# Kernel optimization log

Measured on AMD Instinct MI355X. Metric: run time of the kernel, lower is better.

Reference implementation:

```python
import jax, jax.numpy as jnp
import numpy as np

B, S, D, H = 8, 512, 1024, 16
DH = D // H
GAMMA = 0.1      # kl_gamma
KL_EPS = 1e-10
LN_EPS = 1e-5
SCALE = 1.0 / np.sqrt(DH).astype(np.float32)


def setup_inputs() -> dict:
    key = jax.random.key(0)
    ks = iter(jax.random.split(key, 32))
    rnd = lambda shape, s: jax.random.normal(next(ks), shape, jnp.float32) * s
    inp = {
        'title_features': rnd((B, S, D), 1.0),
        'content_features': rnd((B, S, D), 1.0),
    }
    for pre in ('t2c', 'c2t'):
        # small Q/K weights + bias 1.0 keep row-means of scores positive (log is defined)
        inp[pre + '_wq'] = rnd((D, D), 0.02); inp[pre + '_bq'] = jnp.ones((D,), jnp.float32)
        inp[pre + '_wk'] = rnd((D, D), 0.02); inp[pre + '_bk'] = jnp.ones((D,), jnp.float32)
        inp[pre + '_wv'] = rnd((D, D), 0.02); inp[pre + '_bv'] = jnp.zeros((D,), jnp.float32)
        inp[pre + '_wo'] = rnd((D, D), 0.02); inp[pre + '_bo'] = jnp.zeros((D,), jnp.float32)
    inp['gate_w'] = rnd((2 * D, D), 0.02)
    inp['gate_b'] = jnp.zeros((D,), jnp.float32)
    inp['ln_g'] = jnp.ones((D,), jnp.float32)
    inp['ln_b'] = jnpps = jnp.zeros((D,), jnp.float32)
    inp['ln_b'] = jnp.zeros((D,), jnp.float32)
    return inp


def _daa(q_in, k_in, v_in, wq, bq, wk, bk, wv, bv, wo, bo):
    """DivergenceAlignedAttention forward (eval mode, use_uniform_target=False)."""
    Bq, Sq, _ = q_in.shape
    Sk = k_in.shape[1]
    Q = (q_in @ wq + bq).reshape(Bq, Sq, H, DH)
    K = (k_in @ wk + bk).reshape(Bq, Sk, H, DH)
    V = (v_in @ wv + bv).reshape(Bq, Sk, H, DH)
    scores = jnp.einsum('bqhd,bkhd->bhqk', Q, K) * SCALE           # [B,H,Sq,Sk]
    tgt = jnp.mean(scores, axis=-1, keepdims=True)                 # row mean
    scores = scores + GAMMA * jnp.log(tgt + KL_EPS)                # fused KL term
    attn = jax.nn.softmax(scores, axis=-1)
    ctx = jnp.einsum('bhqk,bkhd->bqhd', attn, V).reshape(Bq, Sq, D)
    return ctx @ wo + bo


def _layer_norm(x, g, b):
    mu = jnp.mean(x, axis=-1, keepdims=True)
    var = jnp.mean(jnp.square(x - mu), axis=-1, keepdims=True)
    return g * (x - mu) / jnp.sqrt(var + LN_EPS) + b


def reference(title_features, content_features,
              t2c_wq, t2c_bq, t2c_wk, t2c_bk, t2c_wv, t2c_bv, t2c_wo, t2c_bo,
              c2t_wq, c2t_bq, c2t_wk, c2t_bk, c2t_wv, c2t_bv, c2t_wo, c2t_bo,
              gate_w, gate_b, ln_g, ln_b):
    t2c = _daa(content_features, title_features, title_features,
               t2c_wq, t2c_bq, t2c_wk, t2c_bk, t2c_wv, t2c_bv, t2c_wo, t2c_bo)
    c2t = _daa(title_features, content_features, content_features,
               c2t_wq, c2t_bq, c2t_wk, c2t_bk, c2t_wv, c2t_bv, c2t_wo, c2t_bo)
    gate_t = jax.nn.sigmoid(jnp.concatenate([title_features, t2c], axis=-1) @ gate_w + gate_b)
    gate_c = jax.nn.sigmoid(jnp.concatenate([content_features, c2t], axis=-1) @ gate_w + gate_b)
    fused_title = _layer_norm(gate_t * title_features + (1.0 - gate_t) * t2c, ln_g, ln_b)
    fused_content = _layer_norm(gate_c * content_features + (1.0 - gate_c) * c2t, ln_g, ln_b)
    return (fused_title, fused_content)
```

## Files before the change

### kernel.cpp

```cpp
#include <hip/hip_runtime.h>
#include <cstdint>
#include <cstddef>

typedef unsigned short ushort_t;
typedef unsigned int u32;
typedef __attribute__((ext_vector_type(8))) short bf16x8;
typedef __attribute__((ext_vector_type(4))) short bf16x4;
typedef __attribute__((ext_vector_type(4))) float f32x4;
typedef __attribute__((ext_vector_type(4))) unsigned short u16x4;

#define DEV static __device__ __forceinline__

DEV ushort_t f2bf(float f) {
  u32 x = __float_as_uint(f);
  x += 0x7fff + ((x >> 16) & 1);
  return (ushort_t)(x >> 16);
}
DEV float bf2f(ushort_t u) { return __uint_as_float(((u32)u) << 16); }

DEV u32 cvtpk(float a, float b) {
  u32 r;
  asm("v_cvt_pk_bf16_f32 %0, %1, %2" : "=v"(r) : "v"(a), "v"(b));
  return r;
}

DEV void gload16(const ushort_t* g, ushort_t* l) {
  __builtin_amdgcn_global_load_lds(
      (const __attribute__((address_space(1))) void*)g,
      (__attribute__((address_space(3))) void*)l, 16, 0, 0);
}


__global__ __launch_bounds__(256) void cvt_inputs(
    const float* __restrict__ xa, const float* __restrict__ xb,
    ushort_t* __restrict__ oa, ushort_t* __restrict__ ob) {
  int i = blockIdx.x * 256 + threadIdx.x;
  f32x4 va = ((const f32x4*)xa)[i];
  f32x4 vb = ((const f32x4*)xb)[i];
  u16x4 ua, ub;
#pragma unroll
  for (int j = 0; j < 4; ++j) { ua[j] = f2bf(va[j]); ub[j] = f2bf(vb[j]); }
  ((u16x4*)oa)[i] = ua;
  ((u16x4*)ob)[i] = ub;
}

struct Src11 { const float* p[11]; };

__global__ __launch_bounds__(256) void transpose_cvt(
    Src11 srcs, ushort_t* __restrict__ WTall, ushort_t* __restrict__ WgT,
    ushort_t* __restrict__ WoBF) {
  const int z = blockIdx.z;
  if (z != 8 && blockIdx.y >= 32) return;
  const float* src = srcs.p[z];
  int tx = threadIdx.x & 31, ty = threadIdx.x >> 5;
  int n0 = blockIdx.x << 5, k0 = blockIdx.y << 5;
  if (z >= 9) {
    ushort_t* dst = WoBF + ((size_t)(z - 9) << 20);
#pragma unroll
    for (int i = 0; i < 4; ++i) {
      size_t off = (size_t)(k0 + ty + i * 8) * 1024 + n0 + tx;
      dst[off] = f2bf(src[off]);
    }
    return;
  }
  const int K = (z == 8) ? 2048 : 1024;
  ushort_t* dst = (z == 8) ? WgT : WTall + ((size_t)z << 20);
  __shared__ float t[32][33];
#pragma unroll
  for (int i = 0; i < 4; ++i)
    t[ty + i * 8][tx] = src[(size_t)(k0 + ty + i * 8) * 1024 + n0 + tx];
  __syncthreads();
#pragma unroll
  for (int i = 0; i < 4; ++i)
    dst[(size_t)(n0 + ty + i * 8) * K + k0 + tx] = f2bf(t[tx][ty + i * 8]);
}

__global__ __launch_bounds__(256) void gb2_kernel(
    const float* __restrict__ bo0, const float* __restrict__ bo1,
    const ushort_t* __restrict__ WgT, float* __restrict__ gb2) {
  const int wgl = blockIdx.x * 4 + (threadIdx.x >> 6);
  const int lane = threadIdx.x & 63;
  const int dir = wgl >> 10, n = wgl & 1023;
  const float* bo = dir ? bo1 : bo0;
  const ushort_t* wrow = WgT + ((size_t)n << 11) + 1024 + (lane << 4);
  float s = 0.f;
#pragma unroll
  for (int j = 0; j < 16; ++j) s += bo[(lane << 4) + j] * bf2f(wrow[j]);
#pragma unroll
  for (int d = 1; d < 64; d <<= 1) s += __shfl_xor(s, d, 64);
  if (lane == 0) gb2[wgl] = s;
}

__global__ __launch_bounds__(256, 3) void gemm_wp(
    const ushort_t* __restrict__ WgT, const ushort_t* __restrict__ WoBF,
    ushort_t* __restrict__ WpT) {
  __shared__ ushort_t As[128 * 64];
  __shared__ ushort_t Bs[128 * 64];
  const int tid = threadIdx.x;
  const int w = tid >> 6, lane = tid & 63;
  const int g = lane >> 4, c = lane & 15;
  const int wm = (w >> 1) << 6, wn = (w & 1) << 6;
  const int m0 = blockIdx.x << 7, n0 = blockIdx.y << 7;
  const int group = m0 >> 10;
  const int csw = (lane & 7) ^ (lane >> 3);

  f32x4 acc[4][4];
#pragma unroll
  for (int i = 0; i < 4; ++i)
#pragma unroll
    for (int j = 0; j < 4; ++j) acc[i][j] = f32x4{0.f, 0.f, 0.f, 0.f};

  for (int k0 = 0; k0 < 1024; k0 += 64) {
#pragma unroll
    for (int i = 0; i < 4; ++i) {
      const int chunk = (w << 2) + i;
      const int row = (chunk << 3) + (lane >> 3);
      gload16(WgT + ((size_t)((m0 + row) & 1023) << 11) + 1024 + k0 + (csw << 3),
              &As[(size_t)chunk << 9]);
      gload16(WoBF + ((size_t)group << 20) + ((size_t)(n0 + row) << 10) + k0 + (csw << 3),
              &Bs[(size_t)chunk << 9]);
    }
    __syncthreads();
    const int cg = c & 7;
#pragma unroll
    for (int ks = 0; ks < 2; ++ks) {
      bf16x8 af[4], bfr[4];
#pragma unroll
      for (int mi = 0; mi < 4; ++mi)
        af[mi] = *(const bf16x8*)&As[((wm + mi * 16 + c) << 6) +
                                     ((((ks << 2) | g) ^ cg) << 3)];
#pragma unroll
      for (int ni = 0; ni < 4; ++ni)
        bfr[ni] = *(const bf16x8*)&Bs[((wn + ni * 16 + c) << 6) +
                                      ((((ks << 2) | g) ^ cg) << 3)];
#pragma unroll
      for (int mi = 0; mi < 4; ++mi)
#pragma unroll
        for (int ni = 0; ni < 4; ++ni)
          acc[mi][ni] = __builtin_amdgcn_mfma_f32_16x16x32_bf16(
              af[mi], bfr[ni], acc[mi][ni], 0, 0, 0);
    }
    __syncthreads();
  }
#pragma unroll
  for (int ni = 0; ni < 4; ++ni) {
    const int n = n0 + wn + ni * 16 + c;
#pragma unroll
    for (int mi = 0; mi < 4; ++mi) {
      const int mb = m0 + wm + mi * 16 + (g << 2);
      f32x4 a = acc[mi][ni];
#pragma unroll
      for (int r = 0; r < 4; ++r)
        WpT[((size_t)group << 20) + ((size_t)((mb + r) & 1023) << 10) + n] = f2bf(a[r]);
    }
  }
}

enum { M_QKVG = 0, M_OG = 1 };
struct Bias8 { const float* p[8]; };

template <int MODE>
__global__ __launch_bounds__(256, 3) void gemm_kernel(
    const ushort_t* __restrict__ Aa, const ushort_t* __restrict__ Ab,
    const ushort_t* __restrict__ WTall, const ushort_t* __restrict__ WgT,
    const ushort_t* __restrict__ WpT, Bias8 bt, const float* __restrict__ gb2,
    ushort_t* __restrict__ outQ, ushort_t* __restrict__ gt) {
  __shared__ ushort_t smem[16384];
  ushort_t* As = smem;
  ushort_t* Bs = smem + 8192;
  const int tid = threadIdx.x;
  const int w = tid >> 6, lane = tid & 63;
  const int g = lane >> 4, c = lane & 15;
  const int wm = (w >> 1) << 6, wn = (w & 1) << 6;
  const int bid = (int)blockIdx.x;
  const int xcd = bid & 7, idx = bid >> 3;
  const int mt = (xcd << 3) + (idx & 7), nt = idx >> 3;
  const int m0 = mt << 7, n0 = nt << 7;
  const int group = m0 >> 12;
  const int nch = n0 >> 10;
  const int csw = (lane & 7) ^ (lane >> 3);

  const ushort_t* Asrc = (MODE == M_QKVG)
      ? ((group ? Ab : Aa) + ((size_t)(m0 & 4095) << 10))
      : (Aa + ((size_t)group << 22) + ((size_t)(m0 & 4095) << 6));

  const ushort_t* Bb;
  int bstr, bidx = -1;
  if (MODE == M_QKVG) {
    if (nch < 3) {
      bidx = group * 3 + nch;
      Bb = WTall + ((size_t)bidx << 20) + ((size_t)(n0 & 1023) << 10);
      bstr = 1024;
    } else {
      Bb = WgT + ((size_t)(n0 & 1023) << 11);
      bstr = 2048;
    }
  } else {
    if (nch == 0) {
      Bb = WTall + ((size_t)(6 + group) << 20) + ((size_t)n0 << 10);
      bstr = 1024;
    } else {
      Bb = WpT + ((size_t)group << 20) + ((size_t)(n0 & 1023) << 10);
      bstr = 1024;
    }
  }

  f32x4 acc[4][4];
#pragma unroll
  for (int i = 0; i < 4; ++i)
#pragma unroll
    for (int j = 0; j < 4; ++j) acc[i][j] = f32x4{0.f, 0.f, 0.f, 0.f};

  for (int k0 = 0; k0 < 1024; k0 += 64) {
#pragma unroll
    for (int i = 0; i < 4; ++i) {
      const int chunk = (w << 2) + i;
      const int row = (chunk << 3) + (lane >> 3);
      const ushort_t* ap;
      if (MODE == M_QKVG)
        ap = Asrc + ((size_t)row << 10) + k0 + (csw << 3);
      else
        ap = Asrc + ((size_t)(k0 >> 6) << 18) + ((size_t)row << 6) + (csw << 3);
      gload16(ap, &As[(size_t)chunk << 9]);
      gload16(Bb + (size_t)row * bstr + k0 + (csw << 3), &Bs[(size_t)chunk << 9]);
    }
    __syncthreads();
    const int cg = c & 7;
#pragma unroll
    for (int ks = 0; ks < 2; ++ks) {
      bf16x8 af[4], bfr[4];
#pragma unroll
      for (int mi = 0; mi < 4; ++mi)
        af[mi] = *(const bf16x8*)&As[((wm + mi * 16 + c) << 6) +
                                     ((((ks << 2) | g) ^ cg) << 3)];
#pragma unroll
      for (int ni = 0; ni < 4; ++ni)
        bfr[ni] = *(const bf16x8*)&Bs[((wn + ni * 16 + c) << 6) +
                                      ((((ks << 2) | g) ^ cg) << 3)];
#pragma unroll
      for (int mi = 0; mi < 4; ++mi)
#pragma unroll
        for (int ni = 0; ni < 4; ++ni)
          acc[mi][ni] = __builtin_amdgcn_mfma_f32_16x16x32_bf16(
              af[mi], bfr[ni], acc[mi][ni], 0, 0, 0);
    }
    __syncthreads();
  }

  const bool vt_path = (MODE == M_QKVG) && (nch < 3) && (bidx == 1 || bidx == 5);
  if (vt_path) {
#pragma unroll
    for (int ni = 0; ni < 4; ++ni) {
      const int nloc = (n0 + wn + ni * 16 + c) & 1023;
      const float bv = bt.p[bidx][nloc];
      const int h = nloc >> 6, d = nloc & 63;
#pragma unroll
      for (int mi = 0; mi < 4; ++mi) {
        const int mrow = (m0 + wm + mi * 16 + (g << 2)) & 4095;
        const int b = mrow >> 9, s = mrow & 511;
        f32x4 a = acc[mi][ni];
        u16x4 o;
#pragma unroll
        for (int r = 0; r < 4; ++r) o[r] = f2bf(a[r] + bv);
        *(u16x4*)&outQ[((size_t)bidx << 22) +
                       (((size_t)((b * 16 + h) * 64 + d)) << 9) + s] = o;
      }
    }
  } else {
#pragma unroll
    for (int ni = 0; ni < 4; ++ni) {
      const int col = wn + ni * 16 + c;
      const int nloc = (n0 + col) & 1023;
      float bv;
      if (MODE == M_QKVG)
        bv = (nch < 3) ? bt.p[bidx][nloc]
                       : bt.p[6][nloc] + gb2[(group << 10) + nloc];
      else
        bv = (nch == 0) ? bt.p[group][nloc] : 0.f;
#pragma unroll
      for (int mi = 0; mi < 4; ++mi) {
        const int rowb = wm + mi * 16 + (g << 2);
        f32x4 a = acc[mi][ni];
#pragma unroll
        for (int r = 0; r < 4; ++r)
          smem[((rowb + r) << 7) + col] = f2bf(a[r] + bv);
      }
    }
    __syncthreads();
    const int lr = tid >> 4;
    const int lc = (tid & 15) << 3;
    ushort_t* obase;
    size_t rbase;
    if (MODE == M_QKVG) {
      if (nch < 3) { obase = outQ + ((size_t)bidx << 22); rbase = (size_t)(m0 & 4095); }
      else         { obase = gt;                          rbase = (size_t)m0; }
    } else {
      if (nch == 0) { obase = outQ; rbase = (size_t)m0; }
      else          { obase = gt;   rbase = (size_t)m0; }
    }
    const int ncol = (n0 & 1023) + lc;
#pragma unroll
    for (int j = 0; j < 8; ++j) {
      const int row = (j << 4) + lr;
      bf16x8 v = *(const bf16x8*)&smem[(row << 7) + lc];
      *(bf16x8*)&obase[((rbase + row) << 10) + ncol] = v;
    }
  }
}

__global__ __launch_bounds__(256, 4) void attn_kernel(
    const ushort_t* __restrict__ QKV, ushort_t* __restrict__ ctx) {
  __shared__ ushort_t Ks[2][4096];
  __shared__ ushort_t Vs[2][4096];
  const int tid = threadIdx.x, w = tid >> 6, lane = tid & 63;
  const int g = lane >> 4, c = lane & 15, c7 = c & 7;
  const int bid = (int)blockIdx.x;
  const int wid = (bid & 7) * 128 + (bid >> 3);
  const int dir = wid >> 9;
  const int bh = (wid >> 2) & 127, qt = wid & 3;
  const int b = bh >> 4, h = bh & 15;
  const int q0 = (qt << 7) + (w << 4);
  const int qs = dir ? 2 : 3, kslot = dir ? 4 : 0, vslot = dir ? 5 : 1;
  const ushort_t* Qb = QKV + ((size_t)qs << 22) + (((size_t)b << 9) << 10) + (h << 6);
  const ushort_t* Kb = QKV + ((size_t)kslot << 22) + (((size_t)b << 9) << 10) + (h << 6);
  const ushort_t* Vb = QKV + ((size_t)vslot << 22) + ((size_t)bh << 15);

  auto stageK = [&](int bb, int kc) {
#pragma unroll
    for (int i = 0; i < 2; ++i) {
      int idx = tid + (i << 8);
      int r = idx >> 3, sl = idx & 7;
      int cs = sl ^ (r & 7);
      gload16(Kb + ((size_t)((kc << 6) + r) << 10) + (cs << 3), &Ks[bb][idx << 3]);
    }
  };
  auto stageV = [&](int bb, int vc) {
#pragma unroll
    for (int i = 0; i < 2; ++i) {
      int idx = tid + (i << 8);
      int r = idx >> 3, sl = idx & 7;
      int cs = sl ^ (r & 7);
      gload16(Vb + ((size_t)r << 9) + (vc << 6) + (cs << 3), &Vs[bb][idx << 3]);
    }
  };

  bf16x8 qfA0 = *(const bf16x8*)&Qb[((size_t)(q0 + c) << 10) + (g << 3)];
  bf16x8 qfA1 = *(const bf16x8*)&Qb[((size_t)(q0 + c) << 10) + 32 + (g << 3)];
  bf16x8 qfB0 = *(const bf16x8*)&Qb[((size_t)(q0 + 64 + c) << 10) + (g << 3)];
  bf16x8 qfB1 = *(const bf16x8*)&Qb[((size_t)(q0 + 64 + c) << 10) + 32 + (g << 3)];

  const float SC = 0.125f;
  float mA = -1e30f, sumA = 0.f, mB = -1e30f, sumB = 0.f;
  f32x4 paccA[4], paccB[4];
#pragma unroll
  for (int dt = 0; dt < 4; ++dt) {
    paccA[dt] = f32x4{0.f, 0.f, 0.f, 0.f};
    paccB[dt] = f32x4{0.f, 0.f, 0.f, 0.f};
  }

  stageK(0, 0);
  stageV(0, 0);
  __syncthreads();

#pragma unroll
  for (int cc = 0; cc < 8; ++cc) {
    const int buf = cc & 1;
    if (cc < 7) { stageK(buf ^ 1, cc + 1); stageV(buf ^ 1, cc + 1); }

    f32x4 stA[4], stB[4];
    __builtin_amdgcn_s_setprio(1);
#pragma unroll
    for (int t = 0; t < 4; ++t) {
      const ushort_t* base = &Ks[buf][((t << 4) + c) << 6];
      bf16x8 a0 = *(const bf16x8*)&base[(g ^ c7) << 3];
      bf16x8 a1 = *(const bf16x8*)&base[((4 | g) ^ c7) << 3];
      f32x4 zA = {0.f, 0.f, 0.f, 0.f}, zB = {0.f, 0.f, 0.f, 0.f};
      zA = __builtin_amdgcn_mfma_f32_16x16x32_bf16(a0, qfA0, zA, 0, 0, 0);
      zB = __builtin_amdgcn_mfma_f32_16x16x32_bf16(a0, qfB0, zB, 0, 0, 0);
      zA = __builtin_amdgcn_mfma_f32_16x16x32_bf16(a1, qfA1, zA, 0, 0, 0);
      zB = __builtin_amdgcn_mfma_f32_16x16x32_bf16(a1, qfB1, zB, 0, 0, 0);
      stA[t] = zA;
      stB[t] = zB;
    }
    __builtin_amdgcn_s_setprio(0);

    float mxA = fmaxf(fmaxf(stA[0][0], stA[0][1]), fmaxf(stA[0][2], stA[0][3]));
    float mxB = fmaxf(fmaxf(stB[0][0], stB[0][1]), fmaxf(stB[0][2], stB[0][3]));
#pragma unroll
    for (int t = 1; t < 4; ++t) {
      mxA = fmaxf(mxA, fmaxf(fmaxf(stA[t][0], stA[t][1]), fmaxf(stA[t][2], stA[t][3])));
      mxB = fmaxf(mxB, fmaxf(fmaxf(stB[t][0], stB[t][1]), fmaxf(stB[t][2], stB[t][3])));
    }
    mxA = fmaxf(mxA, __shfl_xor(mxA, 16, 64));
    mxB = fmaxf(mxB, __shfl_xor(mxB, 16, 64));
    mxA = fmaxf(mxA, __shfl_xor(mxA, 32, 64));
    mxB = fmaxf(mxB, __shfl_xor(mxB, 32, 64));
    if (!__all(mxA <= mA + 64.f)) {
      const float mn = fmaxf(mA, mxA);
      const float sc = __expf((mA - mn) * SC);
      mA = mn;
      sumA *= sc;
#pragma unroll
      for (int dt = 0; dt < 4; ++dt)
#pragma unroll
        for (int r = 0; r < 4; ++r) paccA[dt][r] *= sc;
    }
    if (!__all(mxB <= mB + 64.f)) {
      const float mn = fmaxf(mB, mxB);
      const float sc = __expf((mB - mn) * SC);
      mB = mn;
      sumB *= sc;
#pragma unroll
      for (int dt = 0; dt < 4; ++dt)
#pragma unroll
        for (int r = 0; r < 4; ++r) paccB[dt][r] *= sc;
    }
    float lsA = 0.f, lsB = 0.f;
#pragma unroll
    for (int t = 0; t < 4; ++t)
#pragma unroll
      for (int r = 0; r < 4; ++r) {
        float pA = __expf((stA[t][r] - mA) * SC);
        float pB = __expf((stB[t][r] - mB) * SC);
        stA[t][r] = pA;
        stB[t][r] = pB;
        lsA += pA;
        lsB += pB;
      }
    lsA += __shfl_xor(lsA, 16, 64);
    lsB += __shfl_xor(lsB, 16, 64);
    lsA += __shfl_xor(lsA, 32, 64);
    lsB += __shfl_xor(lsB, 32, 64);
    sumA += lsA;
    sumB += lsB;

#pragma unroll
    for (int ks = 0; ks < 4; ++ks) {
      union { bf16x4 v; u32 wd[2]; } pbA, pbB;
      pbA.wd[0] = cvtpk(stA[ks][0], stA[ks][1]);
      pbA.wd[1] = cvtpk(stA[ks][2], stA[ks][3]);
      pbB.wd[0] = cvtpk(stB[ks][0], stB[ks][1]);
      pbB.wd[1] = cvtpk(stB[ks][2], stB[ks][3]);
      __builtin_amdgcn_s_setprio(1);
#pragma unroll
      for (int dt = 0; dt < 4; ++dt) {
        const int slot = ((ks << 1) | (g >> 1)) ^ c7;
        bf16x4 av = *(const bf16x4*)
            &Vs[buf][(((dt << 4) + c) << 6) + (slot << 3) + ((g & 1) << 2)];
        asm("v_mfma_f32_16x16x16_bf16 %0, %1, %2, %0"
            : "+v"(paccA[dt]) : "v"(av), "v"(pbA.v));
        asm("v_mfma_f32_16x16x16_bf16 %0, %1, %2, %0"
            : "+v"(paccB[dt]) : "v"(av), "v"(pbB.v));
      }
      __builtin_amdgcn_s_setprio(0);
    }
    __syncthreads();
  }

  const float invA = 1.0f / sumA;
  const float invB = 1.0f / sumB;
  ushort_t* cbA = ctx + ((size_t)dir << 22) + ((size_t)h << 18) +
                  ((size_t)(b * 512 + q0 + c) << 6);
  ushort_t* cbB = cbA + ((size_t)64 << 6);
#pragma unroll
  for (int dt = 0; dt < 4; ++dt) {
    union { u16x4 o; u32 wd[2]; } oa, ob;
    oa.wd[0] = cvtpk(paccA[dt][0] * invA, paccA[dt][1] * invA);
    oa.wd[1] = cvtpk(paccA[dt][2] * invA, paccA[dt][3] * invA);
    ob.wd[0] = cvtpk(paccB[dt][0] * invB, paccB[dt][1] * invB);
    ob.wd[1] = cvtpk(paccB[dt][2] * invB, paccB[dt][3] * invB);
    *(u16x4*)&cbA[(dt << 4) + (g << 2)] = oa.o;
    *(u16x4*)&cbB[(dt << 4) + (g << 2)] = ob.o;
  }
}

__global__ __launch_bounds__(256) void fuse_ln(
    const float* __restrict__ xt, const float* __restrict__ xc,
    const ushort_t* __restrict__ ao, const ushort_t* __restrict__ gt,
    const ushort_t* __restrict__ gp,
    const float* __restrict__ lng, const float* __restrict__ lnb,
    float* __restrict__ out) {
  const int row = blockIdx.x, dir = row >> 12, r = row & 4095;
  const float* x = (dir ? xc : xt) + ((size_t)r << 10);
  const ushort_t* a = ao + ((size_t)row << 10);
  const ushort_t* g1 = gt + ((size_t)row << 10);
  const ushort_t* g2 = gp + ((size_t)row << 10);
  float* o = out + ((size_t)row << 10);
  const int t = threadIdx.x, w = t >> 6, lane = t & 63;
  f32x4 xv = ((const f32x4*)x)[t];
  u16x4 av = ((const u16x4*)a)[t];
  u16x4 gv = ((const u16x4*)g1)[t];
  u16x4 pv = ((const u16x4*)g2)[t];
  f32x4 f;
  float sm = 0.f, sq = 0.f;
#pragma unroll
  for (int j = 0; j < 4; ++j) {
    float gate = 1.f / (1.f + __expf(-(bf2f(gv[j]) + bf2f(pv[j]))));
    float fv = gate * xv[j] + (1.f - gate) * bf2f(av[j]);
    f[j] = fv; sm += fv; sq += fv * fv;
  }
#pragma unroll
  for (int d = 1; d < 64; d <<= 1) {
    sm += __shfl_xor(sm, d, 64);
    sq += __shfl_xor(sq, d, 64);
  }
  __shared__ float ps[8];
  if (lane == 0) { ps[w] = sm; ps[4 + w] = sq; }
  __syncthreads();
  sm = ps[0] + ps[1] + ps[2] + ps[3];
  sq = ps[4] + ps[5] + ps[6] + ps[7];
  const float mu = sm * (1.f / 1024.f);
  const float var = sq * (1.f / 1024.f) - mu * mu;
  const float rstd = rsqrtf(var + 1e-5f);
  f32x4 lg = ((const f32x4*)lng)[t], lb = ((const f32x4*)lnb)[t];
  f32x4 ov;
#pragma unroll
  for (int j = 0; j < 4; ++j) ov[j] = lg[j] * (f[j] - mu) * rstd + lb[j];
  ((f32x4*)o)[t] = ov;
}

extern "C" void kernel_launch(void* const* d_in, const int* in_sizes, int n_in,
                              void* d_out, int out_size, void* d_ws, size_t ws_size,
                              hipStream_t stream) {
  (void)in_sizes; (void)n_in; (void)out_size; (void)ws_size;
  const float* title = (const float*)d_in[0];
  const float* content = (const float*)d_in[1];

  char* ws = (char*)d_ws;
  const size_t MB = 1u << 20;
  ushort_t* Xt    = (ushort_t*)(ws + 0 * MB);
  ushort_t* Xc    = (ushort_t*)(ws + 8 * MB);
  ushort_t* ctx   = (ushort_t*)(ws + 0 * MB);
  ushort_t* WTall = (ushort_t*)(ws + 16 * MB);
  ushort_t* WgT   = (ushort_t*)(ws + 32 * MB);
  ushort_t* QKV   = (ushort_t*)(ws + 36 * MB);
  ushort_t* ao    = (ushort_t*)(ws + 36 * MB);
  ushort_t* gpart = (ushort_t*)(ws + 52 * MB);
  ushort_t* gt    = (ushort_t*)(ws + 84 * MB);
  ushort_t* WoBF  = (ushort_t*)(ws + 100 * MB);
  ushort_t* WpT   = (ushort_t*)(ws + 104 * MB);
  float*    gb2   = (float*)   (ws + 108 * MB);

  cvt_inputs<<<4096, 256, 0, stream>>>(title, content, Xt, Xc);

  Src11 srcs;
  srcs.p[0] = (const float*)d_in[4];  srcs.p[1] = (const float*)d_in[6];
  srcs.p[2] = (const float*)d_in[10]; srcs.p[3] = (const float*)d_in[2];
  srcs.p[4] = (const float*)d_in[12]; srcs.p[5] = (const float*)d_in[14];
  srcs.p[6] = (const float*)d_in[8];  srcs.p[7] = (const float*)d_in[16];
  srcs.p[8] = (const float*)d_in[18];
  srcs.p[9] = (const float*)d_in[8];  srcs.p[10] = (const float*)d_in[16];
  transpose_cvt<<<dim3(32, 64, 11), 256, 0, stream>>>(srcs, WTall, WgT, WoBF);

  gb2_kernel<<<512, 256, 0, stream>>>((const float*)d_in[9], (const float*)d_in[17],
                                      WgT, gb2);
  gemm_wp<<<dim3(16, 8), 256, 0, stream>>>(WgT, WoBF, WpT);

  Bias8 bq;
  bq.p[0] = (const float*)d_in[5];  bq.p[1] = (const float*)d_in[7];
  bq.p[2] = (const float*)d_in[11]; bq.p[3] = (const float*)d_in[3];
  bq.p[4] = (const float*)d_in[13]; bq.p[5] = (const float*)d_in[15];
  bq.p[6] = (const float*)d_in[19]; bq.p[7] = nullptr;
  gemm_kernel<M_QKVG><<<2048, 256, 0, stream>>>(Xt, Xc, WTall, WgT, WpT, bq, gb2,
                                                QKV, gt);

  attn_kernel<<<1024, 256, 0, stream>>>(QKV, ctx);

  Bias8 bo;
  bo.p[0] = (const float*)d_in[9]; bo.p[1] = (const float*)d_in[17];
  for (int i = 2; i < 8; ++i) bo.p[i] = nullptr;
  gemm_kernel<M_OG><<<1024, 256, 0, stream>>>(ctx, nullptr, WTall, WgT, WpT, bo, gb2,
                                              ao, gpart);

  fuse_ln<<<8192, 256, 0, stream>>>(title, content, ao, gt, gpart,
                                    (const float*)d_in[20], (const float*)d_in[21],
                                    (float*)d_out);
}
```

Measured before the change: 208.3 us.

## Read K and V fragments directly from global memory in attention kernel

Removes the double-buffered LDS staging of K and V tiles, along with the swizzled shared-memory reads and per-chunk barriers, from the attention kernel. Each wave now loads its MFMA operand fragments straight from global memory (via L1/L2). This drops LDS usage and synchronisation, which may raise occupancy. In exchange, the four waves in a block each fetch the same K/V data, and the loads no longer overlap with compute through prefetching, so the kernel now depends on cache hit rates and global load latency.

```diff
diff --git a/kernel.cpp b/kernel.cpp
--- a/kernel.cpp
+++ b/kernel.cpp
@@ -310,10 +310,8 @@
 
 __global__ __launch_bounds__(256, 4) void attn_kernel(
     const ushort_t* __restrict__ QKV, ushort_t* __restrict__ ctx) {
-  __shared__ ushort_t Ks[2][4096];
-  __shared__ ushort_t Vs[2][4096];
   const int tid = threadIdx.x, w = tid >> 6, lane = tid & 63;
-  const int g = lane >> 4, c = lane & 15, c7 = c & 7;
+  const int g = lane >> 4, c = lane & 15;
   const int bid = (int)blockIdx.x;
   const int wid = (bid & 7) * 128 + (bid >> 3);
   const int dir = wid >> 9;
@@ -325,25 +323,6 @@
   const ushort_t* Kb = QKV + ((size_t)kslot << 22) + (((size_t)b << 9) << 10) + (h << 6);
   const ushort_t* Vb = QKV + ((size_t)vslot << 22) + ((size_t)bh << 15);
 
-  auto stageK = [&](int bb, int kc) {
-#pragma unroll
-    for (int i = 0; i < 2; ++i) {
-      int idx = tid + (i << 8);
-      int r = idx >> 3, sl = idx & 7;
-      int cs = sl ^ (r & 7);
-      gload16(Kb + ((size_t)((kc << 6) + r) << 10) + (cs << 3), &Ks[bb][idx << 3]);
-    }
-  };
-  auto stageV = [&](int bb, int vc) {
-#pragma unroll
-    for (int i = 0; i < 2; ++i) {
-      int idx = tid + (i << 8);
-      int r = idx >> 3, sl = idx & 7;
-      int cs = sl ^ (r & 7);
-      gload16(Vb + ((size_t)r << 9) + (vc << 6) + (cs << 3), &Vs[bb][idx << 3]);
-    }
-  };
-
   bf16x8 qfA0 = *(const bf16x8*)&Qb[((size_t)(q0 + c) << 10) + (g << 3)];
   bf16x8 qfA1 = *(const bf16x8*)&Qb[((size_t)(q0 + c) << 10) + 32 + (g << 3)];
   bf16x8 qfB0 = *(const bf16x8*)&Qb[((size_t)(q0 + 64 + c) << 10) + (g << 3)];
@@ -358,22 +337,15 @@
     paccB[dt] = f32x4{0.f, 0.f, 0.f, 0.f};
   }
 
-  stageK(0, 0);
-  stageV(0, 0);
-  __syncthreads();
-
 #pragma unroll
   for (int cc = 0; cc < 8; ++cc) {
-    const int buf = cc & 1;
-    if (cc < 7) { stageK(buf ^ 1, cc + 1); stageV(buf ^ 1, cc + 1); }
-
     f32x4 stA[4], stB[4];
     __builtin_amdgcn_s_setprio(1);
 #pragma unroll
     for (int t = 0; t < 4; ++t) {
-      const ushort_t* base = &Ks[buf][((t << 4) + c) << 6];
-      bf16x8 a0 = *(const bf16x8*)&base[(g ^ c7) << 3];
-      bf16x8 a1 = *(const bf16x8*)&base[((4 | g) ^ c7) << 3];
+      const ushort_t* krow = Kb + ((size_t)((cc << 6) + (t << 4) + c) << 10);
+      bf16x8 a0 = *(const bf16x8*)&krow[g << 3];
+      bf16x8 a1 = *(const bf16x8*)&krow[32 + (g << 3)];
       f32x4 zA = {0.f, 0.f, 0.f, 0.f}, zB = {0.f, 0.f, 0.f, 0.f};
       zA = __builtin_amdgcn_mfma_f32_16x16x32_bf16(a0, qfA0, zA, 0, 0, 0);
       zB = __builtin_amdgcn_mfma_f32_16x16x32_bf16(a0, qfB0, zB, 0, 0, 0);
@@ -444,9 +416,8 @@
       __builtin_amdgcn_s_setprio(1);
 #pragma unroll
       for (int dt = 0; dt < 4; ++dt) {
-        const int slot = ((ks << 1) | (g >> 1)) ^ c7;
         bf16x4 av = *(const bf16x4*)
-            &Vs[buf][(((dt << 4) + c) << 6) + (slot << 3) + ((g & 1) << 2)];
+            &Vb[(((size_t)(dt << 4) + c) << 9) + (cc << 6) + (ks << 4) + (g << 2)];
         asm("v_mfma_f32_16x16x16_bf16 %0, %1, %2, %0"
             : "+v"(paccA[dt]) : "v"(av), "v"(pbA.v));
         asm("v_mfma_f32_16x16x16_bf16 %0, %1, %2, %0"
@@ -454,7 +425,6 @@
       }
       __builtin_amdgcn_s_setprio(0);
     }
-    __syncthreads();
   }
 
   const float invA = 1.0f / sumA;
```

Result: slower. 265.4 us (+27.4%).
